# Performance work log

Hardware: AMD Instinct MI355X
Metric: run time of the kernel (lower is better)

The kernel has to match this reference:

```python
import jax, jax.numpy as jnp
import numpy as np

N_NODES = 100000
N_HYPEREDGES = 20000
N_INC = 1600000
NFEAT = 256
NCLASS = 64

def setup_inputs() -> dict:
    key = jax.random.key(0)
    k1, k2, k3, k4 = jax.random.split(key, 4)
    x = jax.random.normal(k1, (N_NODES, NFEAT), dtype=jnp.float32)
    node_idx = jax.random.randint(k2, (N_INC,), 0, N_NODES)
    edge_idx = jax.random.randint(k3, (N_INC,), 0, N_HYPEREDGES)
    adj = jnp.stack([node_idx, edge_idx], axis=0)  # [2, N_INC] hyperedge incidence list
    W = jax.random.normal(k4, (NFEAT, NCLASS), dtype=jnp.float32) / np.sqrt(NFEAT).astype(np.float32)
    b = jnp.zeros((NCLASS,), dtype=jnp.float32)
    return {"x": x, "adj": adj, "W": W, "b": b}

def reference(x, adj, W, b):
    # HypergraphConv: out = D^{-1} H B^{-1} H^T (x W) + b, then ReLU
    node_idx = adj[0]  # [E] node index of each incidence
    edge_idx = adj[1]  # [E] hyperedge index of each incidence
    xw = x @ W  # [N, C]

    ones = jnp.ones(node_idx.shape[0], dtype=xw.dtype)
    D = jax.ops.segment_sum(ones, node_idx, num_segments=N_NODES)        # node degree
    Dinv = jnp.where(D > 0, 1.0 / D, 0.0)
    B = jax.ops.segment_sum(ones, edge_idx, num_segments=N_HYPEREDGES)   # hyperedge degree
    Binv = jnp.where(B > 0, 1.0 / B, 0.0)

    # node -> hyperedge aggregation, normalized by B^{-1}
    e_feat = jax.ops.segment_sum(xw[node_idx], edge_idx, num_segments=N_HYPEREDGES) * Binv[:, None]
    # hyperedge -> node aggregation, normalized by D^{-1}
    out = jax.ops.segment_sum(e_feat[edge_idx], node_idx, num_segments=N_NODES) * Dinv[:, None]
    out = out + b
    return jax.nn.relu(out)
```

## Files before the change

### kernel.cpp

```cpp
#include <hip/hip_runtime.h>

#define N_NODES 100000
#define N_EDGES 20000
#define N_INC   1600000
#define NFEAT   256
#define NCLASS  64

#define ELOC 2500
#define NLOC 12500
#define BCAP 201728
#define EPB  8
#define LCAP 192

typedef int v4i __attribute__((ext_vector_type(4)));

__global__ __launch_bounds__(256) void k_bucket(const int* __restrict__ nidx,
                                                const int* __restrict__ eidx,
                                                unsigned int* __restrict__ ebkt,
                                                unsigned int* __restrict__ nbkt,
                                                int* __restrict__ bcur) {
    __shared__ unsigned int stage[16][LCAP];
    __shared__ int lcnt[16];
    __shared__ int gbase[16];
    const int t = threadIdx.x;
    if (t < 16) lcnt[t] = 0;
    __syncthreads();

    const int base = blockIdx.x * 1024 + t * 4;
    if (base < N_INC) {
        const v4i e4 = __builtin_nontemporal_load((const v4i*)&eidx[base]);
        const v4i n4 = __builtin_nontemporal_load((const v4i*)&nidx[base]);
        const int es[4] = {e4.x, e4.y, e4.z, e4.w};
        const int ns[4] = {n4.x, n4.y, n4.z, n4.w};
        #pragma unroll
        for (int q = 0; q < 4; ++q) {
            const int e = es[q], n = ns[q];
            {
                const int b = e & 7;
                const unsigned int pay = ((unsigned int)n << 12) | (unsigned int)(e >> 3);
                const int pos = atomicAdd(&lcnt[b], 1);
                if (pos < LCAP) stage[b][pos] = pay;
                else ebkt[(size_t)b * BCAP + atomicAdd(&bcur[b], 1)] = pay;
            }
            {
                const int b = 8 + (n & 7);
                const unsigned int pay = ((unsigned int)e << 14) | (unsigned int)(n >> 3);
                const int pos = atomicAdd(&lcnt[b], 1);
                if (pos < LCAP) stage[b][pos] = pay;
                else nbkt[(size_t)(b - 8) * BCAP + atomicAdd(&bcur[b], 1)] = pay;
            }
        }
    }
    __syncthreads();
    if (t < 16) gbase[t] = atomicAdd(&bcur[t], min(lcnt[t], LCAP));
    __syncthreads();
    #pragma unroll 1
    for (int k = 0; k < 16; ++k) {
        const int cnt = min(lcnt[k], LCAP);
        const int gb  = gbase[k];
        unsigned int* dst = (k < 8) ? &ebkt[(size_t)k * BCAP]
                                    : &nbkt[(size_t)(k - 8) * BCAP];
        for (int i = t; i < cnt; i += 256) dst[gb + i] = stage[k][i];
    }
}

__global__ __launch_bounds__(256) void k_hist(const unsigned int* __restrict__ bkt,
                                              const int* __restrict__ bcur,
                                              int cur_off,
                                              unsigned short* __restrict__ hist,
                                              int SZ, unsigned int mask) {
    extern __shared__ unsigned int h[];
    const int r = blockIdx.x & 7, b = blockIdx.x >> 3;
    const int t = threadIdx.x;
    for (int i = t; i < SZ; i += 256) h[i] = 0;
    __syncthreads();
    const int cnt = bcur[cur_off + r];
    const int sz  = (cnt + EPB - 1) / EPB;
    const int lo  = b * sz, hi = min(lo + sz, cnt);
    const unsigned int* B = &bkt[(size_t)r * BCAP];
    for (int i = lo + t; i < hi; i += 256)
        atomicAdd(&h[B[i] & mask], 1u);
    __syncthreads();
    unsigned short* H = &hist[(size_t)(r * EPB + b) * SZ];
    for (int i = t; i < SZ; i += 256) H[i] = (unsigned short)h[i];
}

__global__ __launch_bounds__(256) void k_colscan(unsigned short* __restrict__ hist,
                                                 int* __restrict__ cnt_perm, int SZ) {
    const int g = blockIdx.x * 256 + threadIdx.x;
    if (g >= 8 * SZ) return;
    const int r = g / SZ, i = g - r * SZ;
    unsigned short* H = hist + (size_t)r * EPB * SZ + i;
    unsigned int run = 0;
    #pragma unroll
    for (int b = 0; b < EPB; ++b) {
        const unsigned int v = H[(size_t)b * SZ];
        H[(size_t)b * SZ] = (unsigned short)run;
        run += v;
    }
    cnt_perm[g] = (int)run;
}

__global__ __launch_bounds__(1024) void k_scan(const int* __restrict__ cnt,
                                               int* __restrict__ off, int n) {
    __shared__ int part[1024];
    const int t = threadIdx.x;
    const int chunk = ((n / 4 + 1023) / 1024) * 4;
    const int lo = min(t * chunk, n);
    const int hi = min(lo + chunk, n);
    int s = 0;
    for (int i = lo; i < hi; i += 4) {
        const int4 v = *(const int4*)&cnt[i];
        s += v.x + v.y + v.z + v.w;
    }
    part[t] = s;
    __syncthreads();
    for (int d = 1; d < 1024; d <<= 1) {
        int v = (t >= d) ? part[t - d] : 0;
        __syncthreads();
        part[t] += v;
        __syncthreads();
    }
    int run = (t == 0) ? 0 : part[t - 1];
    for (int i = lo; i < hi; i += 4) {
        const int4 v = *(const int4*)&cnt[i];
        int4 o;
        o.x = run; run += v.x;
        o.y = run; run += v.y;
        o.z = run; run += v.z;
        o.w = run; run += v.w;
        *(int4*)&off[i] = o;
    }
}

__global__ __launch_bounds__(256) void k_fill3n(const unsigned int* __restrict__ nbkt,
                                                const int* __restrict__ bcur,
                                                const unsigned short* __restrict__ nhist,
                                                const int* __restrict__ noff,
                                                unsigned short* __restrict__ ninc) {
    __shared__ unsigned int lb[NLOC];
    const int r = blockIdx.x & 7, b = blockIdx.x >> 3;
    const int t = threadIdx.x;
    const unsigned short* H = &nhist[(size_t)(r * EPB + b) * NLOC];
    const int* O = &noff[r * NLOC];
    for (int i = t; i < NLOC; i += 256) lb[i] = (unsigned int)O[i] + H[i];
    __syncthreads();
    const int cnt = bcur[8 + r];
    const int sz  = (cnt + EPB - 1) / EPB;
    const int lo  = b * sz, hi = min(lo + sz, cnt);
    const unsigned int* B = &nbkt[(size_t)r * BCAP];
    for (int i = lo + t; i < hi; i += 256) {
        const unsigned int u = B[i];
        const unsigned int pos = atomicAdd(&lb[u & 0x3FFFu], 1u);
        ninc[pos] = (unsigned short)(u >> 14);
    }
}

__global__ __launch_bounds__(256) void k_fill3e(const unsigned int* __restrict__ ebkt,
                                                const int* __restrict__ bcur,
                                                const unsigned short* __restrict__ ehist,
                                                const int* __restrict__ eoff,
                                                int* __restrict__ einc) {
    __shared__ unsigned int lb[ELOC];
    const int r = blockIdx.x & 7, b = blockIdx.x >> 3;
    const int t = threadIdx.x;
    const unsigned short* H = &ehist[(size_t)(r * EPB + b) * ELOC];
    const int* O = &eoff[r * ELOC];
    for (int i = t; i < ELOC; i += 256) lb[i] = (unsigned int)O[i] + H[i];
    __syncthreads();
    const int cnt = bcur[r];
    const int sz  = (cnt + EPB - 1) / EPB;
    const int lo  = b * sz, hi = min(lo + sz, cnt);
    const unsigned int* B = &ebkt[(size_t)r * BCAP];
    for (int i = lo + t; i < hi; i += 256) {
        const unsigned int u = B[i];
        const unsigned int pos = atomicAdd(&lb[u & 0xFFFu], 1u);
        einc[pos] = (int)(u >> 12);
    }
}

__global__ __launch_bounds__(256) void k_gemm(const float* __restrict__ x,
                                              const float* __restrict__ W,
                                              float* __restrict__ xw) {
    __shared__ __align__(16) float xsT[32][260];
    __shared__ __align__(16) float Wl[32][64];
    const int t  = threadIdx.x;
    const int tr = t >> 3;
    const int tc = (t & 7) * 8;
    const int r0 = blockIdx.x * 256;
    const int q  = t & 7;

    float acc[8][8] = {};

    for (int k0 = 0; k0 < NFEAT; k0 += 32) {
        {
            const float4* src = (const float4*)&W[(size_t)k0 * NCLASS];
            float4* dst = (float4*)&Wl[0][0];
            dst[t]       = src[t];
            dst[t + 256] = src[t + 256];
        }
        #pragma unroll
        for (int it = 0; it < 8; ++it) {
            const int row  = (t >> 3) + it * 32;
            const int grow = r0 + row;
            float4 v = make_float4(0.f, 0.f, 0.f, 0.f);
            if (grow < N_NODES)
                v = *(const float4*)&x[(size_t)grow * NFEAT + k0 + q * 4];
            xsT[q * 4 + 0][row] = v.x;
            xsT[q * 4 + 1][row] = v.y;
            xsT[q * 4 + 2][row] = v.z;
            xsT[q * 4 + 3][row] = v.w;
        }
        __syncthreads();

        #pragma unroll
        for (int kk = 0; kk < 32; ++kk) {
            float xv[8], wv[8];
            *(float4*)&xv[0] = *(const float4*)&xsT[kk][tr * 8];
            *(float4*)&xv[4] = *(const float4*)&xsT[kk][tr * 8 + 4];
            *(float4*)&wv[0] = *(const float4*)&Wl[kk][tc];
            *(float4*)&wv[4] = *(const float4*)&Wl[kk][tc + 4];
            #pragma unroll
            for (int i = 0; i < 8; ++i)
                #pragma unroll
                for (int j = 0; j < 8; ++j)
                    acc[i][j] = fmaf(xv[i], wv[j], acc[i][j]);
        }
        __syncthreads();
    }

    #pragma unroll
    for (int i = 0; i < 8; ++i) {
        const int r = r0 + tr * 8 + i;
        if (r < N_NODES) {
            *(float4*)&xw[(size_t)r * NCLASS + tc]     = *(float4*)&acc[i][0];
            *(float4*)&xw[(size_t)r * NCLASS + tc + 4] = *(float4*)&acc[i][4];
        }
    }
}

__global__ __launch_bounds__(256) void k_edge_gather(const int* __restrict__ einc,
                                                     const int* __restrict__ eoff,
                                                     const int* __restrict__ ecnt,
                                                     const float* __restrict__ xw,
                                                     float* __restrict__ e_feat) {
    const int wave = (blockIdx.x * 256 + threadIdx.x) >> 6;
    const int lane = threadIdx.x & 63;
    if (wave >= N_EDGES) return;
    const int idx  = (wave & 7) * ELOC + (wave >> 3);
    const int base = eoff[idx];
    const int deg  = ecnt[idx];
    float a0 = 0.f, a1 = 0.f, a2 = 0.f, a3 = 0.f;
    int j = base;
    const int end = base + deg;
    for (; j + 4 <= end; j += 4) {
        const int n0 = einc[j], n1 = einc[j + 1], n2 = einc[j + 2], n3 = einc[j + 3];
        a0 += xw[(size_t)n0 * NCLASS + lane];
        a1 += xw[(size_t)n1 * NCLASS + lane];
        a2 += xw[(size_t)n2 * NCLASS + lane];
        a3 += xw[(size_t)n3 * NCLASS + lane];
    }
    for (; j < end; ++j) a0 += xw[(size_t)einc[j] * NCLASS + lane];
    const float s = (a0 + a1) + (a2 + a3);
    e_feat[(size_t)wave * NCLASS + lane] = (deg > 0) ? s / (float)deg : 0.f;
}

__global__ __launch_bounds__(256) void k_node_gather(const unsigned short* __restrict__ ninc,
                                                     const int* __restrict__ noff,
                                                     const int* __restrict__ ncnt,
                                                     const float* __restrict__ e_feat,
                                                     const float* __restrict__ b,
                                                     float* __restrict__ out) {
    const int wave = (blockIdx.x * 256 + threadIdx.x) >> 6;
    const int lane = threadIdx.x & 63;
    if (wave >= N_NODES) return;
    const int idx  = (wave & 7) * NLOC + (wave >> 3);
    const int base = noff[idx];
    const int deg  = ncnt[idx];
    float a0 = 0.f, a1 = 0.f, a2 = 0.f, a3 = 0.f;
    int j = base;
    const int end = base + deg;
    for (; j + 4 <= end; j += 4) {
        const int e0 = ninc[j], e1 = ninc[j + 1], e2 = ninc[j + 2], e3 = ninc[j + 3];
        a0 += e_feat[(size_t)e0 * NCLASS + lane];
        a1 += e_feat[(size_t)e1 * NCLASS + lane];
        a2 += e_feat[(size_t)e2 * NCLASS + lane];
        a3 += e_feat[(size_t)e3 * NCLASS + lane];
    }
    for (; j < end; ++j) a0 += e_feat[(size_t)ninc[j] * NCLASS + lane];
    const float s = (a0 + a1) + (a2 + a3);
    const float r = (deg > 0) ? s / (float)deg : 0.f;
    out[(size_t)wave * NCLASS + lane] = fmaxf(r + b[lane], 0.f);
}

extern "C" void kernel_launch(void* const* d_in, const int* in_sizes, int n_in,
                              void* d_out, int out_size, void* d_ws, size_t ws_size,
                              hipStream_t stream) {
    const float* x    = (const float*)d_in[0];
    const int*   adj  = (const int*)d_in[1];
    const float* W    = (const float*)d_in[2];
    const float* bias = (const float*)d_in[3];
    const int* nidx = adj;
    const int* eidx = adj + N_INC;
    float* out = (float*)d_out;

    char* ws = (char*)d_ws;
    unsigned int*   ebkt  = (unsigned int*)(ws);
    unsigned int*   nbkt  = (unsigned int*)(ws + 6455296);
    unsigned short* ninc  = (unsigned short*)(ws + 12910592);
    unsigned short* nhist = (unsigned short*)(ws + 16110592);
    unsigned short* ehist = (unsigned short*)(ws + 17710592);
    int* ncnt = (int*)(ws + 18030592);
    int* noff = (int*)(ws + 18430592);
    int* ecnt = (int*)(ws + 18830592);
    int* eoff = (int*)(ws + 18910592);
    int* bcur = (int*)(ws + 18990592);
    int*   einc   = (int*)(ws + 6455296);
    float* e_feat = (float*)(ws);

    hipMemsetAsync(bcur, 0, 64, stream);

    k_bucket<<<(N_INC + 1023) / 1024, 256, 0, stream>>>(nidx, eidx, ebkt, nbkt, bcur);

    k_hist<<<8 * EPB, 256, ELOC * 4, stream>>>(ebkt, bcur, 0, ehist, ELOC, 0xFFFu);
    k_hist<<<8 * EPB, 256, NLOC * 4, stream>>>(nbkt, bcur, 8, nhist, NLOC, 0x3FFFu);

    k_colscan<<<(8 * ELOC + 255) / 256, 256, 0, stream>>>(ehist, ecnt, ELOC);
    k_colscan<<<(8 * NLOC + 255) / 256, 256, 0, stream>>>(nhist, ncnt, NLOC);
    k_scan<<<1, 1024, 0, stream>>>(ecnt, eoff, N_EDGES);
    k_scan<<<1, 1024, 0, stream>>>(ncnt, noff, N_NODES);

    k_fill3n<<<8 * EPB, 256, 0, stream>>>(nbkt, bcur, nhist, noff, ninc);
    k_fill3e<<<8 * EPB, 256, 0, stream>>>(ebkt, bcur, ehist, eoff, einc);

    k_gemm<<<(N_NODES + 255) / 256, 256, 0, stream>>>(x, W, out);

    k_edge_gather<<<(N_EDGES * 64) / 256, 256, 0, stream>>>(einc, eoff, ecnt, out, e_feat);

    k_node_gather<<<(N_NODES * 64) / 256, 256, 0, stream>>>(ninc, noff, ncnt, e_feat, bias, out);
}
```

Baseline: 546.3 us.

## Compute x@W with split-bf16 MFMA (3-pass) instead of FP32 FMA

Replaces the scalar FP32 FMA GEMM with a matrix-core GEMM. Both x and W are split into high and low bf16 parts, and three MFMA passes (hh, hl, lh) recover near-FP32 accuracy. A small pre-kernel splits and transposes W into workspace, and the GEMM tile is reduced to 128 rows per block. The GEMM is a modest part of total time, which is dominated by the bucketing and gather kernels. The change trades extra conversion work and a slightly different rounding error for higher matrix throughput.

```diff
diff --git a/kernel.cpp b/kernel.cpp
--- a/kernel.cpp
+++ b/kernel.cpp
@@ -13,6 +13,18 @@
 #define LCAP 192
 
 typedef int v4i __attribute__((ext_vector_type(4)));
+typedef __attribute__((ext_vector_type(8))) short bf16x8;
+typedef __attribute__((ext_vector_type(4))) float f32x4;
+
+__device__ __forceinline__ unsigned short bf16_rne(float f) {
+    unsigned int u = __builtin_bit_cast(unsigned int, f);
+    unsigned int r = (u + 0x7FFFu + ((u >> 16) & 1u)) >> 16;
+    return (unsigned short)r;
+}
+__device__ __forceinline__ float bf16_f(unsigned short h) {
+    unsigned int u = (unsigned int)h << 16;
+    return __builtin_bit_cast(float, u);
+}
 
 __global__ __launch_bounds__(256) void k_bucket(const int* __restrict__ nidx,
                                                 const int* __restrict__ eidx,
@@ -179,62 +191,95 @@
     }
 }
 
+__global__ __launch_bounds__(256) void k_wsplit(const float* __restrict__ W,
+                                                unsigned short* __restrict__ wt_h,
+                                                unsigned short* __restrict__ wt_l) {
+    const int i = blockIdx.x * 256 + threadIdx.x;
+    if (i >= NFEAT * NCLASS) return;
+    const int k = i >> 6, c = i & 63;
+    const float w = W[i];
+    const unsigned short h = bf16_rne(w);
+    wt_h[c * NFEAT + k] = h;
+    wt_l[c * NFEAT + k] = bf16_rne(w - bf16_f(h));
+}
+
 __global__ __launch_bounds__(256) void k_gemm(const float* __restrict__ x,
-                                              const float* __restrict__ W,
+                                              const unsigned short* __restrict__ wt_h,
+                                              const unsigned short* __restrict__ wt_l,
                                               float* __restrict__ xw) {
-    __shared__ __align__(16) float xsT[32][260];
-    __shared__ __align__(16) float Wl[32][64];
-    const int t  = threadIdx.x;
-    const int tr = t >> 3;
-    const int tc = (t & 7) * 8;
-    const int r0 = blockIdx.x * 256;
-    const int q  = t & 7;
-
-    float acc[8][8] = {};
+    __shared__ unsigned short xh[128][40], xl[128][40];
+    __shared__ unsigned short wh[64][40],  wl[64][40];
+    const int t = threadIdx.x;
+    const int wave = t >> 6, lane = t & 63;
+    const int r0 = blockIdx.x * 128;
+    const int fr = lane & 15, fs = lane >> 4;
+
+    f32x4 acc[2][4] = {};
 
     for (int k0 = 0; k0 < NFEAT; k0 += 32) {
-        {
-            const float4* src = (const float4*)&W[(size_t)k0 * NCLASS];
-            float4* dst = (float4*)&Wl[0][0];
-            dst[t]       = src[t];
-            dst[t + 256] = src[t + 256];
-        }
-        #pragma unroll
-        for (int it = 0; it < 8; ++it) {
-            const int row  = (t >> 3) + it * 32;
-            const int grow = r0 + row;
+        #pragma unroll
+        for (int it = 0; it < 4; ++it) {
+            const int s = t + it * 256;
+            const int row = s >> 3, q = s & 7;
+            const int gr = r0 + row;
             float4 v = make_float4(0.f, 0.f, 0.f, 0.f);
-            if (grow < N_NODES)
-                v = *(const float4*)&x[(size_t)grow * NFEAT + k0 + q * 4];
-            xsT[q * 4 + 0][row] = v.x;
-            xsT[q * 4 + 1][row] = v.y;
-            xsT[q * 4 + 2][row] = v.z;
-            xsT[q * 4 + 3][row] = v.w;
+            if (gr < N_NODES)
+                v = *(const float4*)&x[(size_t)gr * NFEAT + k0 + q * 4];
+            ushort4 h, l;
+            h.x = bf16_rne(v.x); l.x = bf16_rne(v.x - bf16_f(h.x));
+            h.y = bf16_rne(v.y); l.y = bf16_rne(v.y - bf16_f(h.y));
+            h.z = bf16_rne(v.z); l.z = bf16_rne(v.z - bf16_f(h.z));
+            h.w = bf16_rne(v.w); l.w = bf16_rne(v.w - bf16_f(h.w));
+            *(ushort4*)&xh[row][q * 4] = h;
+            *(ushort4*)&xl[row][q * 4] = l;
+        }
+        #pragma unroll
+        for (int it = 0; it < 2; ++it) {
+            const int s = t + it * 256;
+            const int c = s >> 3, q = s & 7;
+            *(ushort4*)&wh[c][q * 4] = *(const ushort4*)&wt_h[c * NFEAT + k0 + q * 4];
+            *(ushort4*)&wl[c][q * 4] = *(const ushort4*)&wt_l[c * NFEAT + k0 + q * 4];
         }
         __syncthreads();
 
-        #pragma unroll
-        for (int kk = 0; kk < 32; ++kk) {
-            float xv[8], wv[8];
-            *(float4*)&xv[0] = *(const float4*)&xsT[kk][tr * 8];
-            *(float4*)&xv[4] = *(const float4*)&xsT[kk][tr * 8 + 4];
-            *(float4*)&wv[0] = *(const float4*)&Wl[kk][tc];
-            *(float4*)&wv[4] = *(const float4*)&Wl[kk][tc + 4];
+        bf16x8 a_h[2], a_l[2], b_h[4], b_l[4];
+        #pragma unroll
+        for (int rt = 0; rt < 2; ++rt) {
+            const int row = wave * 32 + rt * 16 + fr;
+            a_h[rt] = *(const bf16x8*)&xh[row][fs * 8];
+            a_l[rt] = *(const bf16x8*)&xl[row][fs * 8];
+        }
+        #pragma unroll
+        for (int ct = 0; ct < 4; ++ct) {
+            const int c = ct * 16 + fr;
+            b_h[ct] = *(const bf16x8*)&wh[c][fs * 8];
+            b_l[ct] = *(const bf16x8*)&wl[c][fs * 8];
+        }
+        #pragma unroll
+        for (int rt = 0; rt < 2; ++rt)
             #pragma unroll
-            for (int i = 0; i < 8; ++i)
-                #pragma unroll
-                for (int j = 0; j < 8; ++j)
-                    acc[i][j] = fmaf(xv[i], wv[j], acc[i][j]);
-        }
+            for (int ct = 0; ct < 4; ++ct) {
+                acc[rt][ct] = __builtin_amdgcn_mfma_f32_16x16x32_bf16(
+                    a_h[rt], b_h[ct], acc[rt][ct], 0, 0, 0);
+                acc[rt][ct] = __builtin_amdgcn_mfma_f32_16x16x32_bf16(
+                    a_h[rt], b_l[ct], acc[rt][ct], 0, 0, 0);
+                acc[rt][ct] = __builtin_amdgcn_mfma_f32_16x16x32_bf16(
+                    a_l[rt], b_h[ct], acc[rt][ct], 0, 0, 0);
+            }
         __syncthreads();
     }
 
     #pragma unroll
-    for (int i = 0; i < 8; ++i) {
-        const int r = r0 + tr * 8 + i;
-        if (r < N_NODES) {
-            *(float4*)&xw[(size_t)r * NCLASS + tc]     = *(float4*)&acc[i][0];
-            *(float4*)&xw[(size_t)r * NCLASS + tc + 4] = *(float4*)&acc[i][4];
+    for (int rt = 0; rt < 2; ++rt) {
+        const int grb = r0 + wave * 32 + rt * 16 + (lane >> 4) * 4;
+        #pragma unroll
+        for (int ct = 0; ct < 4; ++ct) {
+            const int c = ct * 16 + (lane & 15);
+            #pragma unroll
+            for (int reg = 0; reg < 4; ++reg) {
+                const int gr = grb + reg;
+                if (gr < N_NODES) xw[(size_t)gr * NCLASS + c] = acc[rt][ct][reg];
+            }
         }
     }
 }
@@ -315,10 +360,14 @@
     int* ecnt = (int*)(ws + 18830592);
     int* eoff = (int*)(ws + 18910592);
     int* bcur = (int*)(ws + 18990592);
+    unsigned short* wt_h = (unsigned short*)(ws + 18990656);
+    unsigned short* wt_l = (unsigned short*)(ws + 19023424);
     int*   einc   = (int*)(ws + 6455296);
     float* e_feat = (float*)(ws);
 
     hipMemsetAsync(bcur, 0, 64, stream);
+
+    k_wsplit<<<(NFEAT * NCLASS + 255) / 256, 256, 0, stream>>>(W, wt_h, wt_l);
 
     k_bucket<<<(N_INC + 1023) / 1024, 256, 0, stream>>>(nidx, eidx, ebkt, nbkt, bcur);
 
@@ -333,7 +382,7 @@
     k_fill3n<<<8 * EPB, 256, 0, stream>>>(nbkt, bcur, nhist, noff, ninc);
     k_fill3e<<<8 * EPB, 256, 0, stream>>>(ebkt, bcur, ehist, eoff, einc);
 
-    k_gemm<<<(N_NODES + 255) / 256, 256, 0, stream>>>(x, W, out);
+    k_gemm<<<(N_NODES + 127) / 128, 256, 0, stream>>>(x, wt_h, wt_l, out);
 
     k_edge_gather<<<(N_EDGES * 64) / 256, 256, 0, stream>>>(einc, eoff, ecnt, out, e_feat);
 
```

Result: faster. 511.4 us (-6.4%).
